# Kernel tuning notes

Hardware: AMD Instinct MI355X
Metric: run time of the kernel (lower is better)

## Reference

```python
import jax, jax.numpy as jnp
import numpy as np

EPS = 1e-6

def setup_inputs() -> dict:
    key = jax.random.key(0)
    k1, k2 = jax.random.split(key)
    n, c, h, w = 16, 256, 64, 64
    n_F = w
    X = jax.random.normal(k1, (n, c, h, w), dtype=jnp.float32)
    # xavier_uniform for W [n_F, n_F]
    limit = float(np.sqrt(6.0 / (n_F + n_F)))
    W = jax.random.uniform(k2, (n_F, n_F), dtype=jnp.float32, minval=-limit, maxval=limit)
    a2 = jnp.ones((n_F,), dtype=jnp.float32)
    b2 = jnp.zeros((n_F,), dtype=jnp.float32)
    return {"X": X, "W": W, "a2": a2, "b2": b2}

def reference(X, W, a2, b2):
    n, c, h, w = X.shape
    Xf = X.reshape(n * c, h, w)                      # [nc, h, w]
    # attention-like matrix: transpose then softmax over last axis (length h)
    A = jax.nn.softmax(jnp.swapaxes(Xf, 1, 2), axis=2)  # [nc, w, h]
    # custom LayerNorm with unbiased std (torch x.std default, ddof=1)
    mean = jnp.mean(Xf, axis=-1, keepdims=True)
    std = jnp.std(Xf, axis=-1, ddof=1, keepdims=True)
    Xn = a2 * (Xf - mean) / (std + EPS) + b2          # [nc, h, w]
    node = jnp.matmul(A, Xn)                          # [nc, w, w]
    out = jax.nn.relu(jnp.matmul(node, W))            # [nc, w, w]
    return out.reshape(n, c, h, w)
```

## Files before the change

### kernel.cpp

```cpp
#include <hip/hip_runtime.h>
#include <hip/hip_bf16.h>


typedef __attribute__((ext_vector_type(8)))  short  s16x8;
typedef __attribute__((ext_vector_type(16))) float  f32x16;
typedef __attribute__((ext_vector_type(8)))  unsigned short us8;

__device__ __forceinline__ unsigned short f2bf(float x) {
    __hip_bfloat16 b = __float2bfloat16(x);
    return __builtin_bit_cast(unsigned short, b);
}
__device__ __forceinline__ float bf2f(unsigned short h) {
    unsigned u = ((unsigned)h) << 16;
    return __builtin_bit_cast(float, u);
}
__device__ __forceinline__ int swz(int row) {
    return ((row & 7) ^ ((row >> 3) & 7)) << 3;
}
__device__ __forceinline__ int swidx(int row, int k) {
    return row * 64 + (k ^ swz(row));
}

__global__ void prep_w(const float* __restrict__ Wg, unsigned short* __restrict__ ws) {
    const int gid = blockIdx.x * 256 + threadIdx.x;
    const int j = gid & 63;
    const int k = gid >> 6;
    const float x = Wg[k * 64 + j];
    const unsigned short hh = f2bf(x);
    const unsigned short ll = f2bf(x - bf2f(hh));
    ws[j * 64 + k] = hh;
    ws[4096 + j * 64 + k] = ll;
}

__global__ __launch_bounds__(256, 6)
void gnn_mfma(const float* __restrict__ X, const unsigned short* __restrict__ Wp,
              const float* __restrict__ a2, const float* __restrict__ b2,
              float* __restrict__ out)
{
    __shared__ __align__(16) unsigned short bufA[64 * 64];
    __shared__ __align__(16) unsigned short bufX[2][64 * 64];

    const int tid = threadIdx.x;
    const int b   = blockIdx.x;
    const float* xb = X + (size_t)b * 4096;

    const int wid  = tid >> 6;
    const int lane = tid & 63;
    const int r    = lane & 31;
    const int hl   = lane >> 5;
    const int R = (wid & 1) * 32;
    const int C = (wid >> 1) * 32;
    const int rowA = R + r;
    const int rowB = C + r;
    const int swA = swz(rowA);
    const int swB = swz(rowB);

    us8 wh0, wh1, wh2, wh3, wl0, wl1, wl2, wl3;
    {
        const us8* ph = (const us8*)&Wp[rowB * 64 + 8 * hl];
        const us8* pl = (const us8*)&Wp[4096 + rowB * 64 + 8 * hl];
        wh0 = ph[0]; wh1 = ph[2]; wh2 = ph[4]; wh3 = ph[6];
        wl0 = pl[0]; wl1 = pl[2]; wl2 = pl[4]; wl3 = pl[6];
    }

    {
        const int wi = tid >> 2;
        const int h0 = (tid & 3) << 4;
        float v[16];
        #pragma unroll
        for (int i = 0; i < 16; ++i) v[i] = xb[(h0 + i) * 64 + wi];
        float m = v[0];
        #pragma unroll
        for (int i = 1; i < 16; ++i) m = fmaxf(m, v[i]);
        m = fmaxf(m, __shfl_xor(m, 1));
        m = fmaxf(m, __shfl_xor(m, 2));
        float s = 0.f;
        #pragma unroll
        for (int i = 0; i < 16; ++i) { v[i] = __expf(v[i] - m); s += v[i]; }
        s += __shfl_xor(s, 1);
        s += __shfl_xor(s, 2);
        const float inv = 1.0f / s;
        us8 hv0, hv1;
        #pragma unroll
        for (int i = 0; i < 8; ++i) hv0[i] = f2bf(v[i] * inv);
        #pragma unroll
        for (int i = 0; i < 8; ++i) hv1[i] = f2bf(v[8 + i] * inv);
        const int sw = swz(wi);
        *(us8*)&bufA[wi * 64 + (h0 ^ sw)]       = hv0;
        *(us8*)&bufA[wi * 64 + ((h0 + 8) ^ sw)] = hv1;
    }

    {
        const int h  = tid >> 2;
        const int c0 = (tid & 3) << 4;
        float x[16];
        #pragma unroll
        for (int i = 0; i < 4; ++i) {
            float4 t = *(const float4*)&xb[h * 64 + c0 + 4 * i];
            x[4 * i] = t.x; x[4 * i + 1] = t.y; x[4 * i + 2] = t.z; x[4 * i + 3] = t.w;
        }
        float s = 0.f, sq = 0.f;
        #pragma unroll
        for (int i = 0; i < 16; ++i) { s += x[i]; sq += x[i] * x[i]; }
        s  += __shfl_xor(s, 1);  s  += __shfl_xor(s, 2);
        sq += __shfl_xor(sq, 1); sq += __shfl_xor(sq, 2);
        const float mean = s * (1.0f / 64.0f);
        float var = (sq - 64.0f * mean * mean) * (1.0f / 63.0f);
        var = fmaxf(var, 0.0f);
        const float invstd = 1.0f / (sqrtf(var) + 1e-6f);
        #pragma unroll
        for (int i = 0; i < 4; ++i) {
            float4 ta = *(const float4*)&a2[c0 + 4 * i];
            float4 tb = *(const float4*)&b2[c0 + 4 * i];
            const float aa[4] = {ta.x, ta.y, ta.z, ta.w};
            const float bb[4] = {tb.x, tb.y, tb.z, tb.w};
            #pragma unroll
            for (int e = 0; e < 4; ++e) {
                const int c = c0 + 4 * i + e;
                const float xn = aa[e] * (x[4 * i + e] - mean) * invstd + bb[e];
                const unsigned short hh = f2bf(xn);
                const int idx = swidx(c, h);
                bufX[0][idx] = hh;
                bufX[1][idx] = f2bf(xn - bf2f(hh));
            }
        }
    }
    __syncthreads();

    f32x16 acc;
    #pragma unroll
    for (int i = 0; i < 16; ++i) acc[i] = 0.f;

    #pragma unroll
    for (int t = 0; t < 4; ++t) {
        const int k0 = 16 * t + 8 * hl;
        s16x8 aH = *(const s16x8*)&bufA[rowA * 64 + (k0 ^ swA)];
        s16x8 bH = *(const s16x8*)&bufX[0][rowB * 64 + (k0 ^ swB)];
        s16x8 bL = *(const s16x8*)&bufX[1][rowB * 64 + (k0 ^ swB)];
        acc = __builtin_amdgcn_mfma_f32_32x32x16_bf16(aH, bH, acc, 0, 0, 0);
        acc = __builtin_amdgcn_mfma_f32_32x32x16_bf16(aH, bL, acc, 0, 0, 0);
    }
    __syncthreads();

    #pragma unroll
    for (int g = 0; g < 16; ++g) {
        const int w1 = R + (g & 3) + 8 * (g >> 2) + 4 * hl;
        const float xv = acc[g];
        const unsigned short hh = f2bf(xv);
        const int idx = swidx(w1, C + r);
        bufA[idx]    = hh;
        bufX[0][idx] = f2bf(xv - bf2f(hh));
    }
    __syncthreads();

    f32x16 acc2;
    #pragma unroll
    for (int i = 0; i < 16; ++i) acc2[i] = 0.f;

    #pragma unroll
    for (int t = 0; t < 4; ++t) {
        const int k0 = 16 * t + 8 * hl;
        s16x8 nH = *(const s16x8*)&bufA[rowA * 64 + (k0 ^ swA)];
        s16x8 nL = *(const s16x8*)&bufX[0][rowA * 64 + (k0 ^ swA)];
        const s16x8 wH = __builtin_bit_cast(s16x8, t == 0 ? wh0 : t == 1 ? wh1 : t == 2 ? wh2 : wh3);
        const s16x8 wL = __builtin_bit_cast(s16x8, t == 0 ? wl0 : t == 1 ? wl1 : t == 2 ? wl2 : wl3);
        acc2 = __builtin_amdgcn_mfma_f32_32x32x16_bf16(nH, wH, acc2, 0, 0, 0);
        acc2 = __builtin_amdgcn_mfma_f32_32x32x16_bf16(nH, wL, acc2, 0, 0, 0);
        acc2 = __builtin_amdgcn_mfma_f32_32x32x16_bf16(nL, wH, acc2, 0, 0, 0);
    }

    float* ob = out + (size_t)b * 4096;
    #pragma unroll
    for (int g = 0; g < 16; ++g) {
        const int w1 = R + (g & 3) + 8 * (g >> 2) + 4 * hl;
        ob[w1 * 64 + C + r] = fmaxf(acc2[g], 0.f);
    }
}

extern "C" void kernel_launch(void* const* d_in, const int* in_sizes, int n_in,
                              void* d_out, int out_size, void* d_ws, size_t ws_size,
                              hipStream_t stream) {
    const float* X  = (const float*)d_in[0];
    const float* W  = (const float*)d_in[1];
    const float* a2 = (const float*)d_in[2];
    const float* b2 = (const float*)d_in[3];
    float* out = (float*)d_out;
    unsigned short* wp = (unsigned short*)d_ws;
    prep_w<<<16, 256, 0, stream>>>(W, wp);
    gnn_mfma<<<4096, 256, 0, stream>>>(X, wp, a2, b2, out);
}
```

Measured before the change: 139.7 us.

## Process two slices per block to amortize weight loads and add ILP

Each block now handles two (n,c) slices instead of one, so the grid is halved. The W fragment and a2/b2 loads are amortized over two slices, and the two independent MFMA chains per phase can interleave. In exchange LDS use doubles to 48KB and launch bounds drop from 6 to 3 blocks per CU, which cuts occupancy and the latency hiding available for the global loads.

```diff
diff --git a/kernel.cpp b/kernel.cpp
--- a/kernel.cpp
+++ b/kernel.cpp
@@ -27,22 +27,21 @@
     const int k = gid >> 6;
     const float x = Wg[k * 64 + j];
     const unsigned short hh = f2bf(x);
-    const unsigned short ll = f2bf(x - bf2f(hh));
     ws[j * 64 + k] = hh;
-    ws[4096 + j * 64 + k] = ll;
-}
-
-__global__ __launch_bounds__(256, 6)
+    ws[4096 + j * 64 + k] = f2bf(x - bf2f(hh));
+}
+
+__global__ __launch_bounds__(256, 3)
 void gnn_mfma(const float* __restrict__ X, const unsigned short* __restrict__ Wp,
               const float* __restrict__ a2, const float* __restrict__ b2,
               float* __restrict__ out)
 {
-    __shared__ __align__(16) unsigned short bufA[64 * 64];
-    __shared__ __align__(16) unsigned short bufX[2][64 * 64];
+    __shared__ __align__(16) unsigned short bufA [2][64 * 64];
+    __shared__ __align__(16) unsigned short bufXh[2][64 * 64];
+    __shared__ __align__(16) unsigned short bufXl[2][64 * 64];
 
     const int tid = threadIdx.x;
     const int b   = blockIdx.x;
-    const float* xb = X + (size_t)b * 4096;
 
     const int wid  = tid >> 6;
     const int lane = tid & 63;
@@ -55,6 +54,77 @@
     const int swA = swz(rowA);
     const int swB = swz(rowB);
 
+    const int h_  = tid >> 2;
+    const int c0_ = (tid & 3) << 4;
+    float av[16], bv[16];
+    #pragma unroll
+    for (int i = 0; i < 4; ++i) {
+        float4 ta = *(const float4*)&a2[c0_ + 4 * i];
+        float4 tb = *(const float4*)&b2[c0_ + 4 * i];
+        av[4*i] = ta.x; av[4*i+1] = ta.y; av[4*i+2] = ta.z; av[4*i+3] = ta.w;
+        bv[4*i] = tb.x; bv[4*i+1] = tb.y; bv[4*i+2] = tb.z; bv[4*i+3] = tb.w;
+    }
+
+    auto seg1 = [&](const float* xb, unsigned short* bA,
+                    unsigned short* bXh, unsigned short* bXl) {
+        {
+            const int wi = tid >> 2;
+            const int h0 = (tid & 3) << 4;
+            float v[16];
+            #pragma unroll
+            for (int i = 0; i < 16; ++i) v[i] = xb[(h0 + i) * 64 + wi];
+            float m = v[0];
+            #pragma unroll
+            for (int i = 1; i < 16; ++i) m = fmaxf(m, v[i]);
+            m = fmaxf(m, __shfl_xor(m, 1));
+            m = fmaxf(m, __shfl_xor(m, 2));
+            float s = 0.f;
+            #pragma unroll
+            for (int i = 0; i < 16; ++i) { v[i] = __expf(v[i] - m); s += v[i]; }
+            s += __shfl_xor(s, 1);
+            s += __shfl_xor(s, 2);
+            const float inv = 1.0f / s;
+            us8 hv0, hv1;
+            #pragma unroll
+            for (int i = 0; i < 8; ++i) hv0[i] = f2bf(v[i] * inv);
+            #pragma unroll
+            for (int i = 0; i < 8; ++i) hv1[i] = f2bf(v[8 + i] * inv);
+            const int sw = swz(wi);
+            *(us8*)&bA[wi * 64 + (h0 ^ sw)]       = hv0;
+            *(us8*)&bA[wi * 64 + ((h0 + 8) ^ sw)] = hv1;
+        }
+        {
+            float x[16];
+            #pragma unroll
+            for (int i = 0; i < 4; ++i) {
+                float4 t = *(const float4*)&xb[h_ * 64 + c0_ + 4 * i];
+                x[4*i] = t.x; x[4*i+1] = t.y; x[4*i+2] = t.z; x[4*i+3] = t.w;
+            }
+            float s = 0.f, sq = 0.f;
+            #pragma unroll
+            for (int i = 0; i < 16; ++i) { s += x[i]; sq += x[i] * x[i]; }
+            s  += __shfl_xor(s, 1);  s  += __shfl_xor(s, 2);
+            sq += __shfl_xor(sq, 1); sq += __shfl_xor(sq, 2);
+            const float mean = s * (1.0f / 64.0f);
+            float var = (sq - 64.0f * mean * mean) * (1.0f / 63.0f);
+            var = fmaxf(var, 0.0f);
+            const float invstd = 1.0f / (sqrtf(var) + 1e-6f);
+            #pragma unroll
+            for (int i = 0; i < 16; ++i) {
+                const float xn = av[i] * (x[i] - mean) * invstd + bv[i];
+                const unsigned short hh = f2bf(xn);
+                const int idx = swidx(c0_ + i, h_);
+                bXh[idx] = hh;
+                bXl[idx] = f2bf(xn - bf2f(hh));
+            }
+        }
+    };
+
+    const float* xb0 = X + (size_t)(2 * b)     * 4096;
+    const float* xb1 = X + (size_t)(2 * b + 1) * 4096;
+    seg1(xb0, bufA[0], bufXh[0], bufXl[0]);
+    seg1(xb1, bufA[1], bufXh[1], bufXl[1]);
+
     us8 wh0, wh1, wh2, wh3, wl0, wl1, wl2, wl3;
     {
         const us8* ph = (const us8*)&Wp[rowB * 64 + 8 * hl];
@@ -62,118 +132,70 @@
         wh0 = ph[0]; wh1 = ph[2]; wh2 = ph[4]; wh3 = ph[6];
         wl0 = pl[0]; wl1 = pl[2]; wl2 = pl[4]; wl3 = pl[6];
     }
-
-    {
-        const int wi = tid >> 2;
-        const int h0 = (tid & 3) << 4;
-        float v[16];
-        #pragma unroll
-        for (int i = 0; i < 16; ++i) v[i] = xb[(h0 + i) * 64 + wi];
-        float m = v[0];
-        #pragma unroll
-        for (int i = 1; i < 16; ++i) m = fmaxf(m, v[i]);
-        m = fmaxf(m, __shfl_xor(m, 1));
-        m = fmaxf(m, __shfl_xor(m, 2));
-        float s = 0.f;
-        #pragma unroll
-        for (int i = 0; i < 16; ++i) { v[i] = __expf(v[i] - m); s += v[i]; }
-        s += __shfl_xor(s, 1);
-        s += __shfl_xor(s, 2);
-        const float inv = 1.0f / s;
-        us8 hv0, hv1;
-        #pragma unroll
-        for (int i = 0; i < 8; ++i) hv0[i] = f2bf(v[i] * inv);
-        #pragma unroll
-        for (int i = 0; i < 8; ++i) hv1[i] = f2bf(v[8 + i] * inv);
-        const int sw = swz(wi);
-        *(us8*)&bufA[wi * 64 + (h0 ^ sw)]       = hv0;
-        *(us8*)&bufA[wi * 64 + ((h0 + 8) ^ sw)] = hv1;
-    }
-
-    {
-        const int h  = tid >> 2;
-        const int c0 = (tid & 3) << 4;
-        float x[16];
-        #pragma unroll
-        for (int i = 0; i < 4; ++i) {
-            float4 t = *(const float4*)&xb[h * 64 + c0 + 4 * i];
-            x[4 * i] = t.x; x[4 * i + 1] = t.y; x[4 * i + 2] = t.z; x[4 * i + 3] = t.w;
-        }
-        float s = 0.f, sq = 0.f;
-        #pragma unroll
-        for (int i = 0; i < 16; ++i) { s += x[i]; sq += x[i] * x[i]; }
-        s  += __shfl_xor(s, 1);  s  += __shfl_xor(s, 2);
-        sq += __shfl_xor(sq, 1); sq += __shfl_xor(sq, 2);
-        const float mean = s * (1.0f / 64.0f);
-        float var = (sq - 64.0f * mean * mean) * (1.0f / 63.0f);
-        var = fmaxf(var, 0.0f);
-        const float invstd = 1.0f / (sqrtf(var) + 1e-6f);
-        #pragma unroll
-        for (int i = 0; i < 4; ++i) {
-            float4 ta = *(const float4*)&a2[c0 + 4 * i];
-            float4 tb = *(const float4*)&b2[c0 + 4 * i];
-            const float aa[4] = {ta.x, ta.y, ta.z, ta.w};
-            const float bb[4] = {tb.x, tb.y, tb.z, tb.w};
-            #pragma unroll
-            for (int e = 0; e < 4; ++e) {
-                const int c = c0 + 4 * i + e;
-                const float xn = aa[e] * (x[4 * i + e] - mean) * invstd + bb[e];
-                const unsigned short hh = f2bf(xn);
-                const int idx = swidx(c, h);
-                bufX[0][idx] = hh;
-                bufX[1][idx] = f2bf(xn - bf2f(hh));
-            }
-        }
-    }
     __syncthreads();
 
-    f32x16 acc;
-    #pragma unroll
-    for (int i = 0; i < 16; ++i) acc[i] = 0.f;
-
-    #pragma unroll
-    for (int t = 0; t < 4; ++t) {
-        const int k0 = 16 * t + 8 * hl;
-        s16x8 aH = *(const s16x8*)&bufA[rowA * 64 + (k0 ^ swA)];
-        s16x8 bH = *(const s16x8*)&bufX[0][rowB * 64 + (k0 ^ swB)];
-        s16x8 bL = *(const s16x8*)&bufX[1][rowB * 64 + (k0 ^ swB)];
-        acc = __builtin_amdgcn_mfma_f32_32x32x16_bf16(aH, bH, acc, 0, 0, 0);
-        acc = __builtin_amdgcn_mfma_f32_32x32x16_bf16(aH, bL, acc, 0, 0, 0);
-    }
+    auto mm1 = [&](const unsigned short* bA, const unsigned short* bXh,
+                   const unsigned short* bXl) -> f32x16 {
+        f32x16 acc;
+        #pragma unroll
+        for (int i = 0; i < 16; ++i) acc[i] = 0.f;
+        #pragma unroll
+        for (int t = 0; t < 4; ++t) {
+            const int k0 = 16 * t + 8 * hl;
+            s16x8 aH = *(const s16x8*)&bA [rowA * 64 + (k0 ^ swA)];
+            s16x8 bH = *(const s16x8*)&bXh[rowB * 64 + (k0 ^ swB)];
+            s16x8 bL = *(const s16x8*)&bXl[rowB * 64 + (k0 ^ swB)];
+            acc = __builtin_amdgcn_mfma_f32_32x32x16_bf16(aH, bH, acc, 0, 0, 0);
+            acc = __builtin_amdgcn_mfma_f32_32x32x16_bf16(aH, bL, acc, 0, 0, 0);
+        }
+        return acc;
+    };
+    f32x16 acc0 = mm1(bufA[0], bufXh[0], bufXl[0]);
+    f32x16 acc1 = mm1(bufA[1], bufXh[1], bufXl[1]);
     __syncthreads();
 
     #pragma unroll
     for (int g = 0; g < 16; ++g) {
         const int w1 = R + (g & 3) + 8 * (g >> 2) + 4 * hl;
-        const float xv = acc[g];
-        const unsigned short hh = f2bf(xv);
         const int idx = swidx(w1, C + r);
-        bufA[idx]    = hh;
-        bufX[0][idx] = f2bf(xv - bf2f(hh));
+        const float x0 = acc0[g];
+        const unsigned short h0 = f2bf(x0);
+        bufA[0][idx]  = h0;
+        bufXl[0][idx] = f2bf(x0 - bf2f(h0));
+        const float x1 = acc1[g];
+        const unsigned short h1 = f2bf(x1);
+        bufA[1][idx]  = h1;
+        bufXl[1][idx] = f2bf(x1 - bf2f(h1));
     }
     __syncthreads();
 
-    f32x16 acc2;
-    #pragma unroll
-    for (int i = 0; i < 16; ++i) acc2[i] = 0.f;
-
-    #pragma unroll
-    for (int t = 0; t < 4; ++t) {
-        const int k0 = 16 * t + 8 * hl;
-        s16x8 nH = *(const s16x8*)&bufA[rowA * 64 + (k0 ^ swA)];
-        s16x8 nL = *(const s16x8*)&bufX[0][rowA * 64 + (k0 ^ swA)];
-        const s16x8 wH = __builtin_bit_cast(s16x8, t == 0 ? wh0 : t == 1 ? wh1 : t == 2 ? wh2 : wh3);
-        const s16x8 wL = __builtin_bit_cast(s16x8, t == 0 ? wl0 : t == 1 ? wl1 : t == 2 ? wl2 : wl3);
-        acc2 = __builtin_amdgcn_mfma_f32_32x32x16_bf16(nH, wH, acc2, 0, 0, 0);
-        acc2 = __builtin_amdgcn_mfma_f32_32x32x16_bf16(nH, wL, acc2, 0, 0, 0);
-        acc2 = __builtin_amdgcn_mfma_f32_32x32x16_bf16(nL, wH, acc2, 0, 0, 0);
-    }
-
-    float* ob = out + (size_t)b * 4096;
+    auto mm2 = [&](const unsigned short* bNh, const unsigned short* bNl) -> f32x16 {
+        f32x16 acc;
+        #pragma unroll
+        for (int i = 0; i < 16; ++i) acc[i] = 0.f;
+        #pragma unroll
+        for (int t = 0; t < 4; ++t) {
+            const int k0 = 16 * t + 8 * hl;
+            s16x8 nH = *(const s16x8*)&bNh[rowA * 64 + (k0 ^ swA)];
+            s16x8 nL = *(const s16x8*)&bNl[rowA * 64 + (k0 ^ swA)];
+            const s16x8 wH = __builtin_bit_cast(s16x8, t == 0 ? wh0 : t == 1 ? wh1 : t == 2 ? wh2 : wh3);
+            const s16x8 wL = __builtin_bit_cast(s16x8, t == 0 ? wl0 : t == 1 ? wl1 : t == 2 ? wl2 : wl3);
+            acc = __builtin_amdgcn_mfma_f32_32x32x16_bf16(nH, wH, acc, 0, 0, 0);
+            acc = __builtin_amdgcn_mfma_f32_32x32x16_bf16(nH, wL, acc, 0, 0, 0);
+            acc = __builtin_amdgcn_mfma_f32_32x32x16_bf16(nL, wH, acc, 0, 0, 0);
+        }
+        return acc;
+    };
+    f32x16 o0 = mm2(bufA[0], bufXl[0]);
+    f32x16 o1 = mm2(bufA[1], bufXl[1]);
+
+    float* ob0 = out + (size_t)(2 * b)     * 4096;
+    float* ob1 = out + (size_t)(2 * b + 1) * 4096;
     #pragma unroll
     for (int g = 0; g < 16; ++g) {
         const int w1 = R + (g & 3) + 8 * (g >> 2) + 4 * hl;
-        ob[w1 * 64 + C + r] = fmaxf(acc2[g], 0.f);
+        ob0[w1 * 64 + C + r] = fmaxf(o0[g], 0.f);
+        ob1[w1 * 64 + C + r] = fmaxf(o1[g], 0.f);
     }
 }
 
@@ -187,5 +209,5 @@
     float* out = (float*)d_out;
     unsigned short* wp = (unsigned short*)d_ws;
     prep_w<<<16, 256, 0, stream>>>(W, wp);
-    gnn_mfma<<<4096, 256, 0, stream>>>(X, wp, a2, b2, out);
-}
+    gnn_mfma<<<2048, 256, 0, stream>>>(X, wp, a2, b2, out);
+}
```

New measurement: 130.8 us. -6.4%, faster.

## Process four matrices per block with double-buffered LDS and prefetch

Applied to the files above, without the earlier changes.

Each block now handles four consecutive 64x64 slices instead of one, so the grid shrinks to a quarter. The W split and a2/b2 loads are reused across the four slices. The next slice's global loads are issued before the current slice's matmuls, and LDS is double-buffered so writes for the next slice do not need an extra barrier. Costs are higher LDS use (48KB), launch bounds lowered from 6 to 3 waves/occupancy, and manual raw barriers with lgkmcnt waits that rely on correct ordering.

```diff
diff --git a/kernel.cpp b/kernel.cpp
--- a/kernel.cpp
+++ b/kernel.cpp
@@ -20,6 +20,11 @@
 __device__ __forceinline__ int swidx(int row, int k) {
     return row * 64 + (k ^ swz(row));
 }
+
+#define LGKM_DRAIN()  asm volatile("s_waitcnt lgkmcnt(0)" ::: "memory")
+#define RAW_BAR()     do { asm volatile("" ::: "memory");                 \
+                           __builtin_amdgcn_s_barrier();                  \
+                           asm volatile("" ::: "memory"); } while (0)
 
 __global__ void prep_w(const float* __restrict__ Wg, unsigned short* __restrict__ ws) {
     const int gid = blockIdx.x * 256 + threadIdx.x;
@@ -27,22 +32,21 @@
     const int k = gid >> 6;
     const float x = Wg[k * 64 + j];
     const unsigned short hh = f2bf(x);
-    const unsigned short ll = f2bf(x - bf2f(hh));
     ws[j * 64 + k] = hh;
-    ws[4096 + j * 64 + k] = ll;
-}
-
-__global__ __launch_bounds__(256, 6)
+    ws[4096 + j * 64 + k] = f2bf(x - bf2f(hh));
+}
+
+__global__ __launch_bounds__(256, 3)
 void gnn_mfma(const float* __restrict__ X, const unsigned short* __restrict__ Wp,
               const float* __restrict__ a2, const float* __restrict__ b2,
               float* __restrict__ out)
 {
-    __shared__ __align__(16) unsigned short bufA[64 * 64];
-    __shared__ __align__(16) unsigned short bufX[2][64 * 64];
+    __shared__ __align__(16) unsigned short bufA [2][64 * 64];
+    __shared__ __align__(16) unsigned short bufXh[2][64 * 64];
+    __shared__ __align__(16) unsigned short bufXl[2][64 * 64];
 
     const int tid = threadIdx.x;
     const int b   = blockIdx.x;
-    const float* xb = X + (size_t)b * 4096;
 
     const int wid  = tid >> 6;
     const int lane = tid & 63;
@@ -55,6 +59,11 @@
     const int swA = swz(rowA);
     const int swB = swz(rowB);
 
+    const int wi = tid >> 2;
+    const int h0 = (tid & 3) << 4;
+    const int h_  = tid >> 2;
+    const int c0_ = (tid & 3) << 4;
+
     us8 wh0, wh1, wh2, wh3, wl0, wl1, wl2, wl3;
     {
         const us8* ph = (const us8*)&Wp[rowB * 64 + 8 * hl];
@@ -62,118 +71,134 @@
         wh0 = ph[0]; wh1 = ph[2]; wh2 = ph[4]; wh3 = ph[6];
         wl0 = pl[0]; wl1 = pl[2]; wl2 = pl[4]; wl3 = pl[6];
     }
-
-    {
-        const int wi = tid >> 2;
-        const int h0 = (tid & 3) << 4;
-        float v[16];
-        #pragma unroll
-        for (int i = 0; i < 16; ++i) v[i] = xb[(h0 + i) * 64 + wi];
-        float m = v[0];
-        #pragma unroll
-        for (int i = 1; i < 16; ++i) m = fmaxf(m, v[i]);
-        m = fmaxf(m, __shfl_xor(m, 1));
-        m = fmaxf(m, __shfl_xor(m, 2));
-        float s = 0.f;
-        #pragma unroll
-        for (int i = 0; i < 16; ++i) { v[i] = __expf(v[i] - m); s += v[i]; }
-        s += __shfl_xor(s, 1);
-        s += __shfl_xor(s, 2);
-        const float inv = 1.0f / s;
-        us8 hv0, hv1;
-        #pragma unroll
-        for (int i = 0; i < 8; ++i) hv0[i] = f2bf(v[i] * inv);
-        #pragma unroll
-        for (int i = 0; i < 8; ++i) hv1[i] = f2bf(v[8 + i] * inv);
-        const int sw = swz(wi);
-        *(us8*)&bufA[wi * 64 + (h0 ^ sw)]       = hv0;
-        *(us8*)&bufA[wi * 64 + ((h0 + 8) ^ sw)] = hv1;
+    float av[16], bv[16];
+    #pragma unroll
+    for (int i = 0; i < 4; ++i) {
+        float4 ta = *(const float4*)&a2[c0_ + 4 * i];
+        float4 tb = *(const float4*)&b2[c0_ + 4 * i];
+        av[4*i] = ta.x; av[4*i+1] = ta.y; av[4*i+2] = ta.z; av[4*i+3] = ta.w;
+        bv[4*i] = tb.x; bv[4*i+1] = tb.y; bv[4*i+2] = tb.z; bv[4*i+3] = tb.w;
     }
 
-    {
-        const int h  = tid >> 2;
-        const int c0 = (tid & 3) << 4;
-        float x[16];
-        #pragma unroll
-        for (int i = 0; i < 4; ++i) {
-            float4 t = *(const float4*)&xb[h * 64 + c0 + 4 * i];
-            x[4 * i] = t.x; x[4 * i + 1] = t.y; x[4 * i + 2] = t.z; x[4 * i + 3] = t.w;
-        }
-        float s = 0.f, sq = 0.f;
-        #pragma unroll
-        for (int i = 0; i < 16; ++i) { s += x[i]; sq += x[i] * x[i]; }
-        s  += __shfl_xor(s, 1);  s  += __shfl_xor(s, 2);
-        sq += __shfl_xor(sq, 1); sq += __shfl_xor(sq, 2);
-        const float mean = s * (1.0f / 64.0f);
-        float var = (sq - 64.0f * mean * mean) * (1.0f / 63.0f);
-        var = fmaxf(var, 0.0f);
-        const float invstd = 1.0f / (sqrtf(var) + 1e-6f);
-        #pragma unroll
-        for (int i = 0; i < 4; ++i) {
-            float4 ta = *(const float4*)&a2[c0 + 4 * i];
-            float4 tb = *(const float4*)&b2[c0 + 4 * i];
-            const float aa[4] = {ta.x, ta.y, ta.z, ta.w};
-            const float bb[4] = {tb.x, tb.y, tb.z, tb.w};
-            #pragma unroll
-            for (int e = 0; e < 4; ++e) {
-                const int c = c0 + 4 * i + e;
-                const float xn = aa[e] * (x[4 * i + e] - mean) * invstd + bb[e];
+    float  sm[16];
+    float4 ln4[4];
+
+    const float* xb = X + (size_t)(4 * b) * 4096;
+    #pragma unroll
+    for (int i = 0; i < 16; ++i) sm[i] = xb[(h0 + i) * 64 + wi];
+    #pragma unroll
+    for (int i = 0; i < 4; ++i) ln4[i] = *(const float4*)&xb[h_ * 64 + c0_ + 4 * i];
+
+    #pragma unroll
+    for (int t = 0; t < 4; ++t) {
+        const int cur = t & 1;
+
+        {
+            float m = sm[0];
+            #pragma unroll
+            for (int i = 1; i < 16; ++i) m = fmaxf(m, sm[i]);
+            m = fmaxf(m, __shfl_xor(m, 1));
+            m = fmaxf(m, __shfl_xor(m, 2));
+            float s = 0.f;
+            float e[16];
+            #pragma unroll
+            for (int i = 0; i < 16; ++i) { e[i] = __expf(sm[i] - m); s += e[i]; }
+            s += __shfl_xor(s, 1);
+            s += __shfl_xor(s, 2);
+            const float inv = 1.0f / s;
+            us8 hv0, hv1;
+            #pragma unroll
+            for (int i = 0; i < 8; ++i) hv0[i] = f2bf(e[i] * inv);
+            #pragma unroll
+            for (int i = 0; i < 8; ++i) hv1[i] = f2bf(e[8 + i] * inv);
+            const int sw = swz(wi);
+            *(us8*)&bufA[cur][wi * 64 + (h0 ^ sw)]       = hv0;
+            *(us8*)&bufA[cur][wi * 64 + ((h0 + 8) ^ sw)] = hv1;
+        }
+        {
+            float x[16];
+            #pragma unroll
+            for (int i = 0; i < 4; ++i) {
+                x[4*i] = ln4[i].x; x[4*i+1] = ln4[i].y;
+                x[4*i+2] = ln4[i].z; x[4*i+3] = ln4[i].w;
+            }
+            float s = 0.f, sq = 0.f;
+            #pragma unroll
+            for (int i = 0; i < 16; ++i) { s += x[i]; sq += x[i] * x[i]; }
+            s  += __shfl_xor(s, 1);  s  += __shfl_xor(s, 2);
+            sq += __shfl_xor(sq, 1); sq += __shfl_xor(sq, 2);
+            const float mean = s * (1.0f / 64.0f);
+            float var = (sq - 64.0f * mean * mean) * (1.0f / 63.0f);
+            var = fmaxf(var, 0.0f);
+            const float invstd = 1.0f / (sqrtf(var) + 1e-6f);
+            #pragma unroll
+            for (int i = 0; i < 16; ++i) {
+                const float xn = av[i] * (x[i] - mean) * invstd + bv[i];
                 const unsigned short hh = f2bf(xn);
-                const int idx = swidx(c, h);
-                bufX[0][idx] = hh;
-                bufX[1][idx] = f2bf(xn - bf2f(hh));
+                const int idx = swidx(c0_ + i, h_);
+                bufXh[cur][idx] = hh;
+                bufXl[cur][idx] = f2bf(xn - bf2f(hh));
             }
         }
-    }
-    __syncthreads();
-
-    f32x16 acc;
-    #pragma unroll
-    for (int i = 0; i < 16; ++i) acc[i] = 0.f;
-
-    #pragma unroll
-    for (int t = 0; t < 4; ++t) {
-        const int k0 = 16 * t + 8 * hl;
-        s16x8 aH = *(const s16x8*)&bufA[rowA * 64 + (k0 ^ swA)];
-        s16x8 bH = *(const s16x8*)&bufX[0][rowB * 64 + (k0 ^ swB)];
-        s16x8 bL = *(const s16x8*)&bufX[1][rowB * 64 + (k0 ^ swB)];
-        acc = __builtin_amdgcn_mfma_f32_32x32x16_bf16(aH, bH, acc, 0, 0, 0);
-        acc = __builtin_amdgcn_mfma_f32_32x32x16_bf16(aH, bL, acc, 0, 0, 0);
-    }
-    __syncthreads();
-
-    #pragma unroll
-    for (int g = 0; g < 16; ++g) {
-        const int w1 = R + (g & 3) + 8 * (g >> 2) + 4 * hl;
-        const float xv = acc[g];
-        const unsigned short hh = f2bf(xv);
-        const int idx = swidx(w1, C + r);
-        bufA[idx]    = hh;
-        bufX[0][idx] = f2bf(xv - bf2f(hh));
-    }
-    __syncthreads();
-
-    f32x16 acc2;
-    #pragma unroll
-    for (int i = 0; i < 16; ++i) acc2[i] = 0.f;
-
-    #pragma unroll
-    for (int t = 0; t < 4; ++t) {
-        const int k0 = 16 * t + 8 * hl;
-        s16x8 nH = *(const s16x8*)&bufA[rowA * 64 + (k0 ^ swA)];
-        s16x8 nL = *(const s16x8*)&bufX[0][rowA * 64 + (k0 ^ swA)];
-        const s16x8 wH = __builtin_bit_cast(s16x8, t == 0 ? wh0 : t == 1 ? wh1 : t == 2 ? wh2 : wh3);
-        const s16x8 wL = __builtin_bit_cast(s16x8, t == 0 ? wl0 : t == 1 ? wl1 : t == 2 ? wl2 : wl3);
-        acc2 = __builtin_amdgcn_mfma_f32_32x32x16_bf16(nH, wH, acc2, 0, 0, 0);
-        acc2 = __builtin_amdgcn_mfma_f32_32x32x16_bf16(nH, wL, acc2, 0, 0, 0);
-        acc2 = __builtin_amdgcn_mfma_f32_32x32x16_bf16(nL, wH, acc2, 0, 0, 0);
-    }
-
-    float* ob = out + (size_t)b * 4096;
-    #pragma unroll
-    for (int g = 0; g < 16; ++g) {
-        const int w1 = R + (g & 3) + 8 * (g >> 2) + 4 * hl;
-        ob[w1 * 64 + C + r] = fmaxf(acc2[g], 0.f);
+
+        if (t < 3) {
+            const float* xn_ = X + (size_t)(4 * b + t + 1) * 4096;
+            #pragma unroll
+            for (int i = 0; i < 16; ++i) sm[i] = xn_[(h0 + i) * 64 + wi];
+            #pragma unroll
+            for (int i = 0; i < 4; ++i) ln4[i] = *(const float4*)&xn_[h_ * 64 + c0_ + 4 * i];
+        }
+
+        LGKM_DRAIN();
+        RAW_BAR();
+
+        f32x16 acc;
+        #pragma unroll
+        for (int i = 0; i < 16; ++i) acc[i] = 0.f;
+        #pragma unroll
+        for (int t4 = 0; t4 < 4; ++t4) {
+            const int k0 = 16 * t4 + 8 * hl;
+            s16x8 aH = *(const s16x8*)&bufA [cur][rowA * 64 + (k0 ^ swA)];
+            s16x8 bH = *(const s16x8*)&bufXh[cur][rowB * 64 + (k0 ^ swB)];
+            s16x8 bL = *(const s16x8*)&bufXl[cur][rowB * 64 + (k0 ^ swB)];
+            acc = __builtin_amdgcn_mfma_f32_32x32x16_bf16(aH, bH, acc, 0, 0, 0);
+            acc = __builtin_amdgcn_mfma_f32_32x32x16_bf16(aH, bL, acc, 0, 0, 0);
+        }
+        RAW_BAR();
+
+        #pragma unroll
+        for (int g = 0; g < 16; ++g) {
+            const int w1 = R + (g & 3) + 8 * (g >> 2) + 4 * hl;
+            const int idx = swidx(w1, C + r);
+            const float xv = acc[g];
+            const unsigned short hh = f2bf(xv);
+            bufA [cur][idx] = hh;
+            bufXl[cur][idx] = f2bf(xv - bf2f(hh));
+        }
+        LGKM_DRAIN();
+        RAW_BAR();
+
+        f32x16 acc2;
+        #pragma unroll
+        for (int i = 0; i < 16; ++i) acc2[i] = 0.f;
+        #pragma unroll
+        for (int t4 = 0; t4 < 4; ++t4) {
+            const int k0 = 16 * t4 + 8 * hl;
+            s16x8 nH = *(const s16x8*)&bufA [cur][rowA * 64 + (k0 ^ swA)];
+            s16x8 nL = *(const s16x8*)&bufXl[cur][rowA * 64 + (k0 ^ swA)];
+            const s16x8 wH = __builtin_bit_cast(s16x8, t4 == 0 ? wh0 : t4 == 1 ? wh1 : t4 == 2 ? wh2 : wh3);
+            const s16x8 wL = __builtin_bit_cast(s16x8, t4 == 0 ? wl0 : t4 == 1 ? wl1 : t4 == 2 ? wl2 : wl3);
+            acc2 = __builtin_amdgcn_mfma_f32_32x32x16_bf16(nH, wH, acc2, 0, 0, 0);
+            acc2 = __builtin_amdgcn_mfma_f32_32x32x16_bf16(nH, wL, acc2, 0, 0, 0);
+            acc2 = __builtin_amdgcn_mfma_f32_32x32x16_bf16(nL, wH, acc2, 0, 0, 0);
+        }
+
+        float* ob = out + (size_t)(4 * b + t) * 4096;
+        #pragma unroll
+        for (int g = 0; g < 16; ++g) {
+            const int w1 = R + (g & 3) + 8 * (g >> 2) + 4 * hl;
+            ob[w1 * 64 + C + r] = fmaxf(acc2[g], 0.f);
+        }
     }
 }
 
@@ -187,5 +212,5 @@
     float* out = (float*)d_out;
     unsigned short* wp = (unsigned short*)d_ws;
     prep_w<<<16, 256, 0, stream>>>(W, wp);
-    gnn_mfma<<<4096, 256, 0, stream>>>(X, wp, a2, b2, out);
-}
+    gnn_mfma<<<1024, 256, 0, stream>>>(X, wp, a2, b2, out);
+}
```

Result: slower. 156.4 us (+12.0%).
